# Optimization experiments

Measured on AMD Instinct MI355X. Metric: run time of the kernel, lower is better.

Reference implementation:

```python
import jax, jax.numpy as jnp
import numpy as np

KS = 11  # conv kernel size, padding = KS//2 -> SAME


def setup_inputs() -> dict:
    key = jax.random.key(0)
    ks = jax.random.split(key, 6)
    B, H, W = 16, 256, 256
    x = jax.random.uniform(ks[0], (B, 1, H, W), jnp.float32)
    # conv_same(1,1,ks=11,bias=False) -> OIHW kernel [1,1,11,11]
    K = jax.random.normal(ks[1], (1, 1, KS, KS), jnp.float32) * (1.0 / KS)
    # rule: Linear(1,10) -> ReLU -> Linear(10,10) -> ReLU -> Linear(10,1), all with bias
    w1 = jax.random.normal(ks[2], (10, 1), jnp.float32) * 0.5
    b1 = jnp.zeros((10,), jnp.float32)
    w2 = jax.random.normal(ks[3], (10, 10), jnp.float32) * 0.3
    b2 = jnp.zeros((10,), jnp.float32)
    w3 = jax.random.normal(ks[4], (1, 10), jnp.float32) * 0.3
    b3 = jnp.zeros((1,), jnp.float32)
    return {"x": x, "K": K, "w1": w1, "b1": b1, "w2": w2, "b2": b2,
            "w3": w3, "b3": b3, "steps": 16}


def reference(x, K, w1, b1, w2, b2, w3, b3, steps):
    # One NCA step: 11x11 single-channel conv -> pointwise 3-layer MLP on the
    # channel dim (Permute makes Linear act per-pixel) -> clipped residual add.
    def step(xc, _):
        out = jax.lax.conv_general_dilated(
            xc, K, window_strides=(1, 1), padding="SAME",
            dimension_numbers=("NCHW", "OIHW", "NCHW"))  # [B,1,H,W]
        v = out[:, 0]                                   # [B,H,W]
        h = jax.nn.relu(v[..., None] * w1[:, 0] + b1)   # [B,H,W,10]
        h = jax.nn.relu(jnp.einsum("bhwi,oi->bhwo", h, w2) + b2)
        y = jnp.einsum("bhwi,oi->bhwo", h, w3) + b3     # [B,H,W,1]
        xn = jnp.clip(xc + jnp.moveaxis(y, -1, 1), 0.0, 1.0)
        return xn, xn

    _, seq = jax.lax.scan(step, x, None, length=steps)
    # torch returns a list [x0, x1, ..., x_steps]; we stack it.
    return jnp.concatenate([x[None], seq], axis=0)  # [steps+1, B, 1, H, W]
```

## Files before the change

kernel.cpp:

```cpp
#include <hip/hip_runtime.h>


#define HH 256
#define WW 256
#define BB 16
#define TH 16
#define TW 64
#define SH (TH + 10)
#define SW (TW + 10)
#define SWP 76
#define SLAB (BB * HH * WW)
#define NSTEPS 16
#define NB 1024

__device__ __forceinline__ void grid_bar(unsigned* cnt, unsigned target) {
    __syncthreads();
    if (threadIdx.x == 0) {
        __threadfence();
        __hip_atomic_fetch_add(cnt, 1u, __ATOMIC_RELAXED, __HIP_MEMORY_SCOPE_AGENT);
        while (__hip_atomic_load(cnt, __ATOMIC_RELAXED, __HIP_MEMORY_SCOPE_AGENT) < target)
            __builtin_amdgcn_s_sleep(1);
        __threadfence();
    }
    __syncthreads();
}

__device__ __forceinline__ void mlp_precompute(
    const float* __restrict__ w1, const float* __restrict__ b1,
    const float* __restrict__ w2, bool& fast, float (&cp)[10], float (&cn)[10]) {
    fast = true;
#pragma unroll
    for (int i = 0; i < 10; ++i) fast = fast && (b1[i] == 0.f);
#pragma unroll
    for (int o = 0; o < 10; ++o) { cp[o] = 0.f; cn[o] = 0.f; }
    if (fast) {
#pragma unroll
        for (int i = 0; i < 10; ++i) {
            float wi = w1[i];
            float p = fmaxf(wi, 0.f), n = fminf(wi, 0.f);
#pragma unroll
            for (int o = 0; o < 10; ++o) {
                cp[o] = fmaf(p, w2[o * 10 + i], cp[o]);
                cn[o] = fmaf(n, w2[o * 10 + i], cn[o]);
            }
        }
    }
}

__device__ __forceinline__ void step_tile(
    const float* __restrict__ img, float* __restrict__ dst, float* __restrict__ t0,
    float* s, int gy0, int gx0, int tid, bool fast,
    const float (&cp)[10], const float (&cn)[10],
    const float* __restrict__ Kk,
    const float* __restrict__ w1, const float* __restrict__ b1,
    const float* __restrict__ w2, const float* __restrict__ b2,
    const float* __restrict__ w3, float b3v) {
    for (int i = tid; i < SH * SW; i += 256) {
        int r = i / SW, c = i - r * SW;
        int gy = gy0 - 5 + r, gx = gx0 - 5 + c;
        float v = 0.f;
        if (gy >= 0 && gy < HH && gx >= 0 && gx < WW) v = img[gy * WW + gx];
        s[r * SWP + c] = v;
    }
    __syncthreads();

    const int tx = tid & 15, ty = tid >> 4;
    const int x0 = tx * 4;

    float acc0 = 0.f, acc1 = 0.f, acc2 = 0.f, acc3 = 0.f;
#pragma unroll
    for (int ky = 0; ky < 11; ++ky) {
        const float* row = &s[(ty + ky) * SWP + x0];
        float win[16];
        *(float4*)(win + 0)  = *(const float4*)(row + 0);
        *(float4*)(win + 4)  = *(const float4*)(row + 4);
        *(float4*)(win + 8)  = *(const float4*)(row + 8);
        *(float2*)(win + 12) = *(const float2*)(row + 12);
#pragma unroll
        for (int kx = 0; kx < 11; ++kx) {
            float kv = Kk[ky * 11 + kx];
            acc0 = fmaf(win[kx + 0], kv, acc0);
            acc1 = fmaf(win[kx + 1], kv, acc1);
            acc2 = fmaf(win[kx + 2], kv, acc2);
            acc3 = fmaf(win[kx + 3], kv, acc3);
        }
    }

    float vacc[4] = {acc0, acc1, acc2, acc3};
    float res[4];
    if (fast) {
#pragma unroll
        for (int p = 0; p < 4; ++p) {
            float v = vacc[p];
            bool pos = (v >= 0.f);
            float y = b3v;
#pragma unroll
            for (int o = 0; o < 10; ++o) {
                float c = pos ? cp[o] : cn[o];
                float a = fmaf(v, c, b2[o]);
                y = fmaf(fmaxf(a, 0.f), w3[o], y);
            }
            float xc = s[(ty + 5) * SWP + x0 + 5 + p];
            res[p] = fminf(fmaxf(xc + y, 0.f), 1.f);
        }
    } else {
#pragma unroll
        for (int p = 0; p < 4; ++p) {
            float v = vacc[p];
            float h1[10];
#pragma unroll
            for (int i = 0; i < 10; ++i)
                h1[i] = fmaxf(fmaf(v, w1[i], b1[i]), 0.f);
            float y = b3v;
#pragma unroll
            for (int o = 0; o < 10; ++o) {
                float a = b2[o];
#pragma unroll
                for (int i = 0; i < 10; ++i)
                    a = fmaf(h1[i], w2[o * 10 + i], a);
                y = fmaf(fmaxf(a, 0.f), w3[o], y);
            }
            float xc = s[(ty + 5) * SWP + x0 + 5 + p];
            res[p] = fminf(fmaxf(xc + y, 0.f), 1.f);
        }
    }

    if (t0) {
        const float* c0 = &s[(ty + 5) * SWP + x0 + 5];
        float* o0 = t0 + (gy0 + ty) * WW + gx0 + x0;
        *(float4*)o0 = make_float4(c0[0], c0[1], c0[2], c0[3]);
    }
    float* orow = dst + (gy0 + ty) * WW + gx0 + x0;
    *(float4*)orow = make_float4(res[0], res[1], res[2], res[3]);
}

__global__ __launch_bounds__(256, 4) void nca_persist(
    const float* __restrict__ x, float* __restrict__ out, unsigned* cnt,
    const float* __restrict__ Kk,
    const float* __restrict__ w1, const float* __restrict__ b1,
    const float* __restrict__ w2, const float* __restrict__ b2,
    const float* __restrict__ w3, const float* __restrict__ b3) {
    __shared__ __align__(16) float s[SH * SWP];
    const int tid = threadIdx.x;
    const int bid = blockIdx.x;
    const int gx0 = (bid & 3) * TW;
    const int gy0 = ((bid >> 2) & 15) * TH;
    const int b   = bid >> 6;
    const float b3v = b3[0];

    bool fast; float cp[10], cn[10];
    mlp_precompute(w1, b1, w2, fast, cp, cn);

    for (int k = 0; k < NSTEPS; ++k) {
        if (k > 0) grid_bar(cnt, (unsigned)(NB * k));
        const float* img = (k == 0 ? x : out + (size_t)k * SLAB) + b * HH * WW;
        float* dst = out + (size_t)(k + 1) * SLAB + b * HH * WW;
        float* t0  = (k == 0) ? out + b * HH * WW : nullptr;
        step_tile(img, dst, t0, s, gy0, gx0, tid, fast, cp, cn,
                  Kk, w1, b1, w2, b2, w3, b3v);
    }
}

__global__ __launch_bounds__(256) void nca_copy_x(const float* __restrict__ x,
                                                  float* __restrict__ out) {
    int i = (blockIdx.x * 256 + threadIdx.x) * 4;
    *(float4*)(out + i) = *(const float4*)(x + i);
}

__global__ __launch_bounds__(256) void nca_step(
    const float* __restrict__ src, float* __restrict__ dst,
    const float* __restrict__ Kk,
    const float* __restrict__ w1, const float* __restrict__ b1,
    const float* __restrict__ w2, const float* __restrict__ b2,
    const float* __restrict__ w3, const float* __restrict__ b3) {
    __shared__ __align__(16) float s[SH * SWP];
    const int tid = threadIdx.x;
    const int b   = blockIdx.z;
    const int gy0 = blockIdx.y * TH;
    const int gx0 = blockIdx.x * TW;
    const float b3v = b3[0];
    bool fast; float cp[10], cn[10];
    mlp_precompute(w1, b1, w2, fast, cp, cn);
    step_tile(src + b * HH * WW, dst + b * HH * WW, nullptr, s, gy0, gx0, tid,
              fast, cp, cn, Kk, w1, b1, w2, b2, w3, b3v);
}

extern "C" void kernel_launch(void* const* d_in, const int* in_sizes, int n_in,
                              void* d_out, int out_size, void* d_ws, size_t ws_size,
                              hipStream_t stream) {
    const float* x  = (const float*)d_in[0];
    const float* Kk = (const float*)d_in[1];
    const float* w1 = (const float*)d_in[2];
    const float* b1 = (const float*)d_in[3];
    const float* w2 = (const float*)d_in[4];
    const float* b2 = (const float*)d_in[5];
    const float* w3 = (const float*)d_in[6];
    const float* b3 = (const float*)d_in[7];
    float* out = (float*)d_out;

    static int maxb = -1;
    if (maxb < 0) {
        if (hipOccupancyMaxActiveBlocksPerMultiprocessor(
                &maxb, (const void*)nca_persist, 256, 0) != hipSuccess)
            maxb = 0;
    }

    if (maxb >= 4 && d_ws != nullptr && ws_size >= 64) {
        hipMemsetAsync(d_ws, 0, 64, stream);
        nca_persist<<<NB, 256, 0, stream>>>(x, out, (unsigned*)d_ws,
                                            Kk, w1, b1, w2, b2, w3, b3);
    } else {
        nca_copy_x<<<SLAB / (256 * 4), 256, 0, stream>>>(x, out);
        dim3 grid(WW / TW, HH / TH, BB);
        for (int k = 0; k < 16; ++k) {
            nca_step<<<grid, 256, 0, stream>>>(out + (size_t)k * SLAB,
                                               out + (size_t)(k + 1) * SLAB,
                                               Kk, w1, b1, w2, b2, w3, b3);
        }
    }
}
```

Baseline: 360.1 us.

## Replace grid-wide barrier with per-tile neighbor flags and XCD-aware tile mapping

Replaces the global atomic-counter barrier between steps with per-tile progress flags. Each block now waits only on its up-to-9 neighboring tiles in the same image before reading the previous step's output. Block indices are remapped so each XCD handles whole images, which keeps neighbor halo data and flags in the same L2. This removes the global serialization and contention on one counter, at the cost of more flag traffic and a larger workspace memset.

New measurement: 363.4 us. About the same (+0.9%).

```diff
diff --git a/kernel.cpp b/kernel.cpp
--- a/kernel.cpp
+++ b/kernel.cpp
@@ -13,18 +13,6 @@
 #define NSTEPS 16
 #define NB 1024
 
-__device__ __forceinline__ void grid_bar(unsigned* cnt, unsigned target) {
-    __syncthreads();
-    if (threadIdx.x == 0) {
-        __threadfence();
-        __hip_atomic_fetch_add(cnt, 1u, __ATOMIC_RELAXED, __HIP_MEMORY_SCOPE_AGENT);
-        while (__hip_atomic_load(cnt, __ATOMIC_RELAXED, __HIP_MEMORY_SCOPE_AGENT) < target)
-            __builtin_amdgcn_s_sleep(1);
-        __threadfence();
-    }
-    __syncthreads();
-}
-
 __device__ __forceinline__ void mlp_precompute(
     const float* __restrict__ w1, const float* __restrict__ b1,
     const float* __restrict__ w2, bool& fast, float (&cp)[10], float (&cn)[10]) {
@@ -135,7 +123,7 @@
 }
 
 __global__ __launch_bounds__(256, 4) void nca_persist(
-    const float* __restrict__ x, float* __restrict__ out, unsigned* cnt,
+    const float* __restrict__ x, float* __restrict__ out, unsigned* flags,
     const float* __restrict__ Kk,
     const float* __restrict__ w1, const float* __restrict__ b1,
     const float* __restrict__ w2, const float* __restrict__ b2,
@@ -143,21 +131,50 @@
     __shared__ __align__(16) float s[SH * SWP];
     const int tid = threadIdx.x;
     const int bid = blockIdx.x;
-    const int gx0 = (bid & 3) * TW;
-    const int gy0 = ((bid >> 2) & 15) * TH;
-    const int b   = bid >> 6;
+
+    const int xcd = bid & 7;
+    const int idx = bid >> 3;
+    const int b   = (xcd << 1) | (idx >> 6);
+    const int rem = idx & 63;
+    const int by  = rem >> 2;
+    const int bx  = rem & 3;
+    const int gy0 = by * TH, gx0 = bx * TW;
+    const int myflag = b * 64 + by * 4 + bx;
+
+    int nbr = -1;
+    if (tid < 9) {
+        int dy = tid / 3 - 1, dx = tid % 3 - 1;
+        int ny = by + dy, nx = bx + dx;
+        if (ny >= 0 && ny < 16 && nx >= 0 && nx < 4)
+            nbr = b * 64 + ny * 4 + nx;
+    }
+
     const float b3v = b3[0];
-
     bool fast; float cp[10], cn[10];
     mlp_precompute(w1, b1, w2, fast, cp, cn);
 
     for (int k = 0; k < NSTEPS; ++k) {
-        if (k > 0) grid_bar(cnt, (unsigned)(NB * k));
+        if (k > 0) {
+            if (nbr >= 0) {
+                while (__hip_atomic_load(&flags[nbr], __ATOMIC_RELAXED,
+                                         __HIP_MEMORY_SCOPE_AGENT) < (unsigned)k)
+                    __builtin_amdgcn_s_sleep(1);
+                __threadfence();
+            }
+            __syncthreads();
+        }
         const float* img = (k == 0 ? x : out + (size_t)k * SLAB) + b * HH * WW;
         float* dst = out + (size_t)(k + 1) * SLAB + b * HH * WW;
         float* t0  = (k == 0) ? out + b * HH * WW : nullptr;
         step_tile(img, dst, t0, s, gy0, gx0, tid, fast, cp, cn,
                   Kk, w1, b1, w2, b2, w3, b3v);
+
+        __syncthreads();
+        if (tid == 0) {
+            __threadfence();
+            __hip_atomic_store(&flags[myflag], (unsigned)(k + 1),
+                               __ATOMIC_RELAXED, __HIP_MEMORY_SCOPE_AGENT);
+        }
     }
 }
 
@@ -205,8 +222,8 @@
             maxb = 0;
     }
 
-    if (maxb >= 4 && d_ws != nullptr && ws_size >= 64) {
-        hipMemsetAsync(d_ws, 0, 64, stream);
+    if (maxb >= 4 && d_ws != nullptr && ws_size >= NB * sizeof(unsigned)) {
+        hipMemsetAsync(d_ws, 0, NB * sizeof(unsigned), stream);
         nca_persist<<<NB, 256, 0, stream>>>(x, out, (unsigned*)d_ws,
                                             Kk, w1, b1, w2, b2, w3, b3);
     } else {
```
